# Performance work log

Hardware: AMD Instinct MI355X
Metric: run time of the kernel (lower is better)

Reference implementation:

```python
import jax, jax.numpy as jnp
import numpy as np

B, T, H = 8, 2048, 1024

def setup_inputs() -> dict:
    key = jax.random.key(0)
    ks = jax.random.split(key, 7)
    s = 1.0 / np.sqrt(H)
    return {
        "x": jax.random.normal(ks[0], (B, T, H), dtype=jnp.float32),
        "Wq": jax.random.uniform(ks[1], (H, H), jnp.float32, -s, s),
        "bq": jax.random.uniform(ks[2], (H,), jnp.float32, -s, s),
        "Wk": jax.random.uniform(ks[3], (H, H), jnp.float32, -s, s),
        "bk": jax.random.uniform(ks[4], (H,), jnp.float32, -s, s),
        "Wv": jax.random.uniform(ks[5], (H, H), jnp.float32, -s, s),
        "bv": jax.random.uniform(ks[6], (H,), jnp.float32, -s, s),
    }

def reference(x, Wq, bq, Wk, bk, Wv, bv):
    # Linear layers: y = x @ W^T + b (torch convention: store W as [out,in]; here square so use [in,out] directly)
    Q = x @ Wq + bq                      # [B, T, H]
    K = x @ Wk + bk
    V = x @ Wv + bv
    scores = jnp.einsum('bqd,bkd->bqk', Q, K) / jnp.sqrt(jnp.float32(x.shape[-1]))
    # NOTE: original uses nn.Softmax(dim=1) -> softmax over the QUERY axis (axis=1)
    attention = jax.nn.softmax(scores, axis=1)  # [B, T, T]
    out = jnp.einsum('bqk,bkd->bqd', attention, V)
    return out
```

## Files before the change

### kernel.cpp

```cpp
#include <hip/hip_runtime.h>
#include <hip/hip_bf16.h>

typedef __attribute__((ext_vector_type(8))) short short8;
typedef __attribute__((ext_vector_type(4))) float f32x4;

__device__ __forceinline__ float bf2f(unsigned short u) {
    unsigned v = ((unsigned)u) << 16;
    float f;
    __builtin_memcpy(&f, &v, 4);
    return f;
}
__device__ __forceinline__ unsigned short f2bf(float f) {
    unsigned v;
    __builtin_memcpy(&v, &f, 4);
    unsigned r = (v + 0x7fffu + ((v >> 16) & 1u)) >> 16;
    return (unsigned short)r;
}

#define GLD16(g, l)                                                            \
    __builtin_amdgcn_global_load_lds(                                          \
        (const __attribute__((address_space(1))) void*)(g),                    \
        (__attribute__((address_space(3))) void*)(l), 16, 0, 0)

__global__ __launch_bounds__(256) void cast_f32_bf16(const float* __restrict__ in,
                                                     unsigned short* __restrict__ out,
                                                     size_t n) {
    size_t stride = (size_t)gridDim.x * blockDim.x * 4;
    for (size_t i = ((size_t)blockIdx.x * blockDim.x + threadIdx.x) * 4; i < n; i += stride) {
        float4 v = *(const float4*)(in + i);
        ushort4 o;
        o.x = f2bf(v.x); o.y = f2bf(v.y); o.z = f2bf(v.z); o.w = f2bf(v.w);
        *(ushort4*)(out + i) = o;
    }
}

__global__ __launch_bounds__(256) void cast_transpose_w(const float* __restrict__ W,
                                                        unsigned short* __restrict__ WT, int D) {
    __shared__ float tile[32][33];
    int bx = blockIdx.x * 32;
    int by = blockIdx.y * 32;
    int tx = threadIdx.x & 31, ty = threadIdx.x >> 5;
    for (int i = 0; i < 32; i += 8)
        tile[ty + i][tx] = W[(size_t)(by + ty + i) * D + bx + tx];
    __syncthreads();
    for (int i = 0; i < 32; i += 8)
        WT[(size_t)(bx + ty + i) * D + by + tx] = f2bf(tile[tx][ty + i]);
}

__global__ __launch_bounds__(256) void concat3(const float* __restrict__ a,
                                               const float* __restrict__ b,
                                               const float* __restrict__ c,
                                               float* __restrict__ o, int n) {
    int i = blockIdx.x * 256 + threadIdx.x;
    if (i < n) { o[i] = a[i]; o[n + i] = b[i]; o[2 * n + i] = c[i]; }
}

template <int EPI, int REMAP>
__global__ __launch_bounds__(512, 2) void gemm256(
    const unsigned short* __restrict__ A, const unsigned short* __restrict__ B,
    void* __restrict__ Cv, const float* __restrict__ bias,
    int K, float scale, int lda, int ldb, int ldc,
    long sA, long sB, long sC) {
    __shared__ __attribute__((aligned(16))) unsigned short sm[2][2][2][8192];

    const int tid = threadIdx.x;
    const int wv = tid >> 6, lane = tid & 63;
    const int wm = wv >> 2, wn = wv & 3;
    const int r16 = lane & 15, cHi = lane >> 4;

    int mt, ntl, bz;
    if (REMAP) {
        int i = blockIdx.x + gridDim.x * (blockIdx.y + gridDim.y * blockIdx.z);
        bz = i & 7;
        int slot = i >> 3;
        ntl = slot % gridDim.x;
        mt = slot / gridDim.x;
    } else {
        bz = blockIdx.z; mt = blockIdx.y; ntl = blockIdx.x;
    }
    const int tileM = mt * 256, tileN = ntl * 256;
    A += (size_t)bz * sA;
    B += (size_t)bz * sB;

    size_t offA[2], offB[2];
    int ldsOff[2];
    const int swzsrc = ((lane & 3) ^ ((lane >> 3) & 3)) * 8;
#pragma unroll
    for (int j = 0; j < 2; ++j) {
        int row = (wv * 2 + j) * 16 + (lane >> 2);
        offA[j] = (size_t)(tileM + row) * lda + swzsrc;
        offB[j] = (size_t)(tileN + row) * ldb + swzsrc;
        ldsOff[j] = (wv * 2 + j) * 1024;
    }

#define STAGE(BUF, P, KT)                                                       \
    do {                                                                        \
        const unsigned short* _s = ((P) & 1) ? B : A;                           \
        const size_t* _o = ((P) & 1) ? offB : offA;                             \
        char* _d = (char*)&sm[BUF][(P) >> 1][(P) & 1][0];                       \
        GLD16(_s + _o[0] + (KT) + ((P) >> 1) * 32, _d + ldsOff[0]);             \
        GLD16(_s + _o[1] + (KT) + ((P) >> 1) * 32, _d + ldsOff[1]);             \
    } while (0)

    f32x4 acc[8][4];
#pragma unroll
    for (int m = 0; m < 8; ++m)
#pragma unroll
        for (int n = 0; n < 4; ++n) acc[m][n] = (f32x4){0.f, 0.f, 0.f, 0.f};

    const int slotXor = (lane >> 1) & 3;
    const int aBase = (wm * 128 + r16) * 32 + (cHi ^ slotXor) * 8;
    const int bBase = (wn * 64 + r16) * 32 + (cHi ^ slotXor) * 8;

    STAGE(0, 0, 0); STAGE(0, 1, 0); STAGE(0, 2, 0); STAGE(0, 3, 0);
    asm volatile("s_waitcnt vmcnt(4)" ::: "memory");
    __builtin_amdgcn_s_barrier();

    short8 aF[8], bF0, bF1;
    const int ktiles = K >> 6;
    for (int t = 0; t < ktiles; ++t) {
        const int cur = t & 1, nxt = cur ^ 1;
        const int ktn = (t + 1 == ktiles) ? 0 : ((t + 1) << 6);
        const unsigned short* A0 = &sm[cur][0][0][0];
        const unsigned short* B0 = &sm[cur][0][1][0];
        const unsigned short* A1 = &sm[cur][1][0][0];
        const unsigned short* B1 = &sm[cur][1][1][0];

#pragma unroll
        for (int m = 0; m < 8; ++m) aF[m] = *(const short8*)&A0[aBase + m * 512];
        bF0 = *(const short8*)&B0[bBase];
        bF1 = *(const short8*)&B0[bBase + 512];
        STAGE(nxt, 0, ktn);
        __builtin_amdgcn_s_barrier();
        asm volatile("s_waitcnt lgkmcnt(0)" ::: "memory");
        __builtin_amdgcn_sched_barrier(0);
        __builtin_amdgcn_s_setprio(1);
#pragma unroll
        for (int m = 0; m < 8; ++m) {
            acc[m][0] = __builtin_amdgcn_mfma_f32_16x16x32_bf16(aF[m], bF0, acc[m][0], 0, 0, 0);
            acc[m][1] = __builtin_amdgcn_mfma_f32_16x16x32_bf16(aF[m], bF1, acc[m][1], 0, 0, 0);
        }
        __builtin_amdgcn_s_setprio(0);
        __builtin_amdgcn_s_barrier();

        bF0 = *(const short8*)&B0[bBase + 1024];
        bF1 = *(const short8*)&B0[bBase + 1536];
        STAGE(nxt, 1, ktn);
        __builtin_amdgcn_s_barrier();
        asm volatile("s_waitcnt lgkmcnt(0)" ::: "memory");
        __builtin_amdgcn_sched_barrier(0);
        __builtin_amdgcn_s_setprio(1);
#pragma unroll
        for (int m = 0; m < 8; ++m) {
            acc[m][2] = __builtin_amdgcn_mfma_f32_16x16x32_bf16(aF[m], bF0, acc[m][2], 0, 0, 0);
            acc[m][3] = __builtin_amdgcn_mfma_f32_16x16x32_bf16(aF[m], bF1, acc[m][3], 0, 0, 0);
        }
        __builtin_amdgcn_s_setprio(0);
        asm volatile("s_waitcnt vmcnt(4)" ::: "memory");
        __builtin_amdgcn_s_barrier();

#pragma unroll
        for (int m = 0; m < 8; ++m) aF[m] = *(const short8*)&A1[aBase + m * 512];
        bF0 = *(const short8*)&B1[bBase];
        bF1 = *(const short8*)&B1[bBase + 512];
        STAGE(nxt, 2, ktn);
        __builtin_amdgcn_s_barrier();
        asm volatile("s_waitcnt lgkmcnt(0)" ::: "memory");
        __builtin_amdgcn_sched_barrier(0);
        __builtin_amdgcn_s_setprio(1);
#pragma unroll
        for (int m = 0; m < 8; ++m) {
            acc[m][0] = __builtin_amdgcn_mfma_f32_16x16x32_bf16(aF[m], bF0, acc[m][0], 0, 0, 0);
            acc[m][1] = __builtin_amdgcn_mfma_f32_16x16x32_bf16(aF[m], bF1, acc[m][1], 0, 0, 0);
        }
        __builtin_amdgcn_s_setprio(0);
        __builtin_amdgcn_s_barrier();

        bF0 = *(const short8*)&B1[bBase + 1024];
        bF1 = *(const short8*)&B1[bBase + 1536];
        STAGE(nxt, 3, ktn);
        __builtin_amdgcn_s_barrier();
        asm volatile("s_waitcnt lgkmcnt(0)" ::: "memory");
        __builtin_amdgcn_sched_barrier(0);
        __builtin_amdgcn_s_setprio(1);
#pragma unroll
        for (int m = 0; m < 8; ++m) {
            acc[m][2] = __builtin_amdgcn_mfma_f32_16x16x32_bf16(aF[m], bF0, acc[m][2], 0, 0, 0);
            acc[m][3] = __builtin_amdgcn_mfma_f32_16x16x32_bf16(aF[m], bF1, acc[m][3], 0, 0, 0);
        }
        __builtin_amdgcn_s_setprio(0);
        asm volatile("s_waitcnt vmcnt(4)" ::: "memory");
        __builtin_amdgcn_s_barrier();
    }
    asm volatile("s_waitcnt vmcnt(0)" ::: "memory");
#undef STAGE

    const int rowB = tileM + wm * 128 + cHi * 4;
    const int colB = tileN + wn * 64 + r16;
#pragma unroll
    for (int m = 0; m < 8; ++m) {
#pragma unroll
        for (int n = 0; n < 4; ++n) {
            const int col = colB + n * 16;
            float badd = (EPI == 0) ? bias[col] : 0.f;
#pragma unroll
            for (int r = 0; r < 4; ++r) {
                int row = rowB + m * 16 + r;
                float v = acc[m][n][r];
                if (EPI == 0) v += badd;
                if (EPI == 1) v = __expf(v * scale);
                size_t idx = (size_t)bz * sC + (size_t)row * ldc + col;
                if (EPI == 2) ((float*)Cv)[idx] = v;
                else ((unsigned short*)Cv)[idx] = f2bf(v);
            }
        }
    }
}

__global__ __launch_bounds__(256) void col_sum_partial(const unsigned short* __restrict__ E,
                                                       float* __restrict__ partial, int T) {
    int b = blockIdx.z;
    int k = blockIdx.x * 256 + threadIdx.x;
    int q0 = blockIdx.y * 64;
    const unsigned short* p = E + (size_t)b * T * T + (size_t)q0 * T + k;
    float sum = 0.f;
#pragma unroll 4
    for (int q = 0; q < 64; ++q)
        sum += bf2f(p[(size_t)q * T]);
    partial[((size_t)b * gridDim.y + blockIdx.y) * T + k] = sum;
}

__global__ __launch_bounds__(256) void col_sum_reduce(const float* __restrict__ partial,
                                                      float* __restrict__ invl, int T, int nchunk) {
    int b = blockIdx.y;
    int k = blockIdx.x * 256 + threadIdx.x;
    float s = 0.f;
    for (int c = 0; c < nchunk; ++c)
        s += partial[((size_t)b * nchunk + c) * T + k];
    invl[(size_t)b * T + k] = 1.0f / s;
}

__global__ __launch_bounds__(256) void transpose_scale_bf16(
    const unsigned short* __restrict__ V, const float* __restrict__ invl,
    unsigned short* __restrict__ Vt, int T, int H, int ldv) {
    __shared__ unsigned short tile[64][66];
    int b = blockIdx.z;
    const unsigned short* Vb = V + (size_t)b * T * ldv;
    unsigned short* Vtb = Vt + (size_t)b * H * T;
    const float* il = invl + (size_t)b * T;
    int x0 = blockIdx.x * 64;
    int y0 = blockIdx.y * 64;
    int t = threadIdx.x;
    for (int i = 0; i < 16; ++i) {
        int idx = t + i * 256;
        int r = idx >> 6, c = idx & 63;
        tile[r][c] = Vb[(size_t)(y0 + r) * ldv + x0 + c];
    }
    __syncthreads();
    for (int i = 0; i < 16; ++i) {
        int idx = t + i * 256;
        int r = idx >> 6, c = idx & 63;
        float v = bf2f(tile[c][r]) * il[y0 + c];
        Vtb[(size_t)(x0 + r) * T + y0 + c] = f2bf(v);
    }
}

extern "C" void kernel_launch(void* const* d_in, const int* in_sizes, int n_in,
                              void* d_out, int out_size, void* d_ws, size_t ws_size,
                              hipStream_t stream) {
    const int B = 8, T = 2048, H = 1024;
    const size_t MT = (size_t)B * T;
    const int H3 = 3 * H;

    const float* x  = (const float*)d_in[0];
    const float* Wq = (const float*)d_in[1];
    const float* bq = (const float*)d_in[2];
    const float* Wk = (const float*)d_in[3];
    const float* bk = (const float*)d_in[4];
    const float* Wv = (const float*)d_in[5];
    const float* bv = (const float*)d_in[6];
    float* out = (float*)d_out;

    char* ws = (char*)d_ws;
    size_t o = 0;
    unsigned short* xb   = (unsigned short*)(ws + o); o += MT * H * 2;
    unsigned short* Wcat = (unsigned short*)(ws + o); o += (size_t)H3 * H * 2;
    float* bcat          = (float*)(ws + o);          o += (size_t)H3 * 4;
    unsigned short* QKVb = (unsigned short*)(ws + o); o += MT * H3 * 2;
    unsigned short* Eb   = (unsigned short*)(ws + o); o += (size_t)B * T * T * 2;
    float* partial       = (float*)(ws + o);          o += (size_t)B * 32 * T * 4;
    float* invl          = (float*)(ws + o);          o += (size_t)B * T * 4;
    unsigned short* Vt   = xb;

    cast_f32_bf16<<<2048, 256, 0, stream>>>(x, xb, MT * H);
    dim3 wgrid(32, 32);
    cast_transpose_w<<<wgrid, 256, 0, stream>>>(Wq, Wcat, H);
    cast_transpose_w<<<wgrid, 256, 0, stream>>>(Wk, Wcat + (size_t)H * H, H);
    cast_transpose_w<<<wgrid, 256, 0, stream>>>(Wv, Wcat + (size_t)2 * H * H, H);
    concat3<<<4, 256, 0, stream>>>(bq, bk, bv, bcat, H);

    gemm256<0, 0><<<dim3(H3 / 256, MT / 256, 1), 512, 0, stream>>>(
        xb, Wcat, QKVb, bcat, H, 1.f, H, H, H3, 0, 0, 0);

    gemm256<1, 1><<<dim3(T / 256, T / 256, B), 512, 0, stream>>>(
        QKVb, QKVb + H, Eb, nullptr, H, 0.03125f, H3, H3, T,
        (long)T * H3, (long)T * H3, (long)T * T);

    col_sum_partial<<<dim3(T / 256, 32, B), 256, 0, stream>>>(Eb, partial, T);
    col_sum_reduce<<<dim3(T / 256, B), 256, 0, stream>>>(partial, invl, T, 32);

    transpose_scale_bf16<<<dim3(H / 64, T / 64, B), 256, 0, stream>>>(
        QKVb + 2 * H, invl, Vt, T, H, H3);

    gemm256<2, 1><<<dim3(H / 256, T / 256, B), 512, 0, stream>>>(
        Eb, Vt, out, nullptr, T, 1.f, T, T, H,
        (long)T * T, (long)H * T, (long)T * H);

    (void)in_sizes; (void)n_in; (void)out_size; (void)ws_size;
}
```

Baseline: 305.4 us.

## Fuse softmax column sums into QK^T GEMM epilogue via atomics; merge weight casts

```diff
diff --git a/kernel.cpp b/kernel.cpp
--- a/kernel.cpp
+++ b/kernel.cpp
@@ -34,9 +34,13 @@
     }
 }
 
-__global__ __launch_bounds__(256) void cast_transpose_w(const float* __restrict__ W,
-                                                        unsigned short* __restrict__ WT, int D) {
+__global__ __launch_bounds__(256) void cast_transpose_w3(const float* __restrict__ W0,
+                                                         const float* __restrict__ W1,
+                                                         const float* __restrict__ W2,
+                                                         unsigned short* __restrict__ WT, int D) {
     __shared__ float tile[32][33];
+    const float* W = (blockIdx.z == 0) ? W0 : (blockIdx.z == 1) ? W1 : W2;
+    unsigned short* dst = WT + (size_t)blockIdx.z * D * D;
     int bx = blockIdx.x * 32;
     int by = blockIdx.y * 32;
     int tx = threadIdx.x & 31, ty = threadIdx.x >> 5;
@@ -44,7 +48,7 @@
         tile[ty + i][tx] = W[(size_t)(by + ty + i) * D + bx + tx];
     __syncthreads();
     for (int i = 0; i < 32; i += 8)
-        WT[(size_t)(bx + ty + i) * D + by + tx] = f2bf(tile[tx][ty + i]);
+        dst[(size_t)(bx + ty + i) * D + by + tx] = f2bf(tile[tx][ty + i]);
 }
 
 __global__ __launch_bounds__(256) void concat3(const float* __restrict__ a,
@@ -55,10 +59,20 @@
     if (i < n) { o[i] = a[i]; o[n + i] = b[i]; o[2 * n + i] = c[i]; }
 }
 
+__global__ __launch_bounds__(256) void zerof(float* __restrict__ p, int n) {
+    int i = blockIdx.x * 256 + threadIdx.x;
+    if (i < n) p[i] = 0.f;
+}
+
+__global__ __launch_bounds__(256) void recipf(float* __restrict__ p, int n) {
+    int i = blockIdx.x * 256 + threadIdx.x;
+    if (i < n) p[i] = 1.0f / p[i];
+}
+
 template <int EPI, int REMAP>
 __global__ __launch_bounds__(512, 2) void gemm256(
     const unsigned short* __restrict__ A, const unsigned short* __restrict__ B,
-    void* __restrict__ Cv, const float* __restrict__ bias,
+    void* __restrict__ Cv, const float* __restrict__ bias, float* __restrict__ csum,
     int K, float scale, int lda, int ldb, int ldc,
     long sA, long sB, long sC) {
     __shared__ __attribute__((aligned(16))) unsigned short sm[2][2][2][8192];
@@ -197,6 +211,7 @@
 
     const int rowB = tileM + wm * 128 + cHi * 4;
     const int colB = tileN + wn * 64 + r16;
+    float cs[4] = {0.f, 0.f, 0.f, 0.f};
 #pragma unroll
     for (int m = 0; m < 8; ++m) {
 #pragma unroll
@@ -208,36 +223,23 @@
                 int row = rowB + m * 16 + r;
                 float v = acc[m][n][r];
                 if (EPI == 0) v += badd;
-                if (EPI == 1) v = __expf(v * scale);
+                if (EPI == 1) { v = __expf(v * scale); cs[n] += v; }
                 size_t idx = (size_t)bz * sC + (size_t)row * ldc + col;
                 if (EPI == 2) ((float*)Cv)[idx] = v;
                 else ((unsigned short*)Cv)[idx] = f2bf(v);
             }
         }
     }
-}
-
-__global__ __launch_bounds__(256) void col_sum_partial(const unsigned short* __restrict__ E,
-                                                       float* __restrict__ partial, int T) {
-    int b = blockIdx.z;
-    int k = blockIdx.x * 256 + threadIdx.x;
-    int q0 = blockIdx.y * 64;
-    const unsigned short* p = E + (size_t)b * T * T + (size_t)q0 * T + k;
-    float sum = 0.f;
-#pragma unroll 4
-    for (int q = 0; q < 64; ++q)
-        sum += bf2f(p[(size_t)q * T]);
-    partial[((size_t)b * gridDim.y + blockIdx.y) * T + k] = sum;
-}
-
-__global__ __launch_bounds__(256) void col_sum_reduce(const float* __restrict__ partial,
-                                                      float* __restrict__ invl, int T, int nchunk) {
-    int b = blockIdx.y;
-    int k = blockIdx.x * 256 + threadIdx.x;
-    float s = 0.f;
-    for (int c = 0; c < nchunk; ++c)
-        s += partial[((size_t)b * nchunk + c) * T + k];
-    invl[(size_t)b * T + k] = 1.0f / s;
+    if (EPI == 1) {
+#pragma unroll
+        for (int n = 0; n < 4; ++n) {
+            float s = cs[n];
+            s += __shfl_xor(s, 16, 64);
+            s += __shfl_xor(s, 32, 64);
+            if (cHi == 0)
+                atomicAdd(&csum[(size_t)bz * ldc + colB + n * 16], s);
+        }
+    }
 }
 
 __global__ __launch_bounds__(256) void transpose_scale_bf16(
@@ -288,32 +290,28 @@
     float* bcat          = (float*)(ws + o);          o += (size_t)H3 * 4;
     unsigned short* QKVb = (unsigned short*)(ws + o); o += MT * H3 * 2;
     unsigned short* Eb   = (unsigned short*)(ws + o); o += (size_t)B * T * T * 2;
-    float* partial       = (float*)(ws + o);          o += (size_t)B * 32 * T * 4;
-    float* invl          = (float*)(ws + o);          o += (size_t)B * T * 4;
+    float* colsum        = (float*)(ws + o);          o += (size_t)B * T * 4;
     unsigned short* Vt   = xb;
 
     cast_f32_bf16<<<2048, 256, 0, stream>>>(x, xb, MT * H);
-    dim3 wgrid(32, 32);
-    cast_transpose_w<<<wgrid, 256, 0, stream>>>(Wq, Wcat, H);
-    cast_transpose_w<<<wgrid, 256, 0, stream>>>(Wk, Wcat + (size_t)H * H, H);
-    cast_transpose_w<<<wgrid, 256, 0, stream>>>(Wv, Wcat + (size_t)2 * H * H, H);
+    cast_transpose_w3<<<dim3(32, 32, 3), 256, 0, stream>>>(Wq, Wk, Wv, Wcat, H);
     concat3<<<4, 256, 0, stream>>>(bq, bk, bv, bcat, H);
+    zerof<<<64, 256, 0, stream>>>(colsum, B * T);
 
     gemm256<0, 0><<<dim3(H3 / 256, MT / 256, 1), 512, 0, stream>>>(
-        xb, Wcat, QKVb, bcat, H, 1.f, H, H, H3, 0, 0, 0);
+        xb, Wcat, QKVb, bcat, nullptr, H, 1.f, H, H, H3, 0, 0, 0);
 
     gemm256<1, 1><<<dim3(T / 256, T / 256, B), 512, 0, stream>>>(
-        QKVb, QKVb + H, Eb, nullptr, H, 0.03125f, H3, H3, T,
+        QKVb, QKVb + H, Eb, nullptr, colsum, H, 0.03125f, H3, H3, T,
         (long)T * H3, (long)T * H3, (long)T * T);
 
-    col_sum_partial<<<dim3(T / 256, 32, B), 256, 0, stream>>>(Eb, partial, T);
-    col_sum_reduce<<<dim3(T / 256, B), 256, 0, stream>>>(partial, invl, T, 32);
+    recipf<<<64, 256, 0, stream>>>(colsum, B * T);
 
     transpose_scale_bf16<<<dim3(H / 64, T / 64, B), 256, 0, stream>>>(
-        QKVb + 2 * H, invl, Vt, T, H, H3);
+        QKVb + 2 * H, colsum, Vt, T, H, H3);
 
     gemm256<2, 1><<<dim3(H / 256, T / 256, B), 512, 0, stream>>>(
-        Eb, Vt, out, nullptr, T, 1.f, T, T, H,
+        Eb, Vt, out, nullptr, nullptr, T, 1.f, T, T, H,
         (long)T * T, (long)H * T, (long)T * H);
 
     (void)in_sizes; (void)n_in; (void)out_size; (void)ws_size;
```

Result: faster. 288.5 us (-5.5%).
